# Kernel optimization log

Hardware: AMD Instinct MI355X
Metric: run time of the kernel (lower is better)

Reference implementation:

```python
import jax, jax.numpy as jnp
import numpy as np

NEURONS = 54
DT = 4
STEPS = 30
POOL = 8

# SpikingNN: forward = (ex > 0).float(); backward = straight-through where ex > 0.
# Combined with nn.functional.threshold(rate, thr, 0), the spike output is
# (rate > thr).float() with gradient d spike/d rate = 1{rate > thr}.
@jax.custom_vjp
def spike(rate, thr):
    return (rate > thr).astype(rate.dtype)

def _spike_fwd(rate, thr):
    mask = rate > thr
    return mask.astype(rate.dtype), mask

def _spike_bwd(mask, g):
    return (g * mask.astype(g.dtype), jnp.zeros((), g.dtype))

spike.defvjp(_spike_fwd, _spike_bwd)

def setup_inputs() -> dict:
    key = jax.random.key(0)
    k1, k2, k3, k4, k5 = jax.random.split(key, 5)
    B = 16
    x = jax.random.normal(k1, (B, STEPS, 600, 600), jnp.float32)
    # small scales keep exp(current_sum) numerically stable
    fc_w = jax.random.normal(k2, (NEURONS, 75 * 75), jnp.float32) * 0.01
    fc_b = jax.random.normal(k3, (NEURONS,), jnp.float32) * 0.01
    l_weight = jax.random.uniform(k4, (NEURONS, DT), jnp.float32) * 0.01
    h_weight = jax.random.uniform(k5, (DT,), jnp.float32) * 0.01
    return {"x": x, "fc_w": fc_w, "fc_b": fc_b, "l_weight": l_weight, "h_weight": h_weight}

def reference(x, fc_w, fc_b, l_weight, h_weight):
    B = x.shape[0]
    H = x.shape[2] // POOL
    W = x.shape[3] // POOL
    # avg_pool2d(x, 8): non-overlapping 8x8 mean -> [B, 30, 75, 75]
    xp = x.reshape(B, STEPS, H, POOL, W, POOL).mean(axis=(3, 5))
    # per-frame fc: [B, 30, 5625] @ [5625, 54]^T + b -> [B, 30, 54]
    frames = jnp.einsum('btp,np->btn', xp.reshape(B, STEPS, H * W), fc_w) + fc_b
    count0 = jnp.zeros((B, NEURONS), x.dtype)
    hist0 = jnp.zeros((B, NEURONS, DT), x.dtype)

    def step(carry, frame):
        count, hist = carry                      # hist: [B, N, DT]
        hsum = hist * l_weight                   # [B, N, DT]
        lateral = hsum.sum(axis=(1, 2))[:, None] - hsum.sum(axis=2)  # [B, N]
        cur = frame + lateral + (hist * h_weight).sum(axis=2)
        rate = jnp.exp(cur)
        thr = jax.lax.stop_gradient(rate.mean())
        s = spike(rate, thr)                     # [B, N]
        hist = jnp.concatenate([hist[:, :, 1:], s[:, :, None]], axis=2)
        return (count + s, hist), None

    (count, _), _ = jax.lax.scan(step, (count0, hist0), jnp.swapaxes(frames, 0, 1))
    return jax.nn.softplus(count)
```

## Files before the change

kernel.cpp:

```cpp
#include <hip/hip_runtime.h>
#include <math.h>

#define NEURONS 54
#define DT 4
#define STEPS 30
#define BATCH 16
#define HW 75
#define P 5625
#define PPAD 5632
#define PPAD4 (PPAD/4)

__global__ void repack_w(const float* __restrict__ fc_w, float* __restrict__ wpad) {
    int idx = blockIdx.x * blockDim.x + threadIdx.x;
    if (idx >= NEURONS * PPAD) return;
    int n = idx / PPAD, p = idx % PPAD;
    wpad[idx] = (p < P) ? fc_w[n * P + p] : 0.0f;
}

__global__ __launch_bounds__(512) void pool_fc(
    const float* __restrict__ x, const float* __restrict__ wpad,
    const float* __restrict__ fc_b, float* __restrict__ frames) {
    __shared__ __align__(16) float xp_s[PPAD];
    __shared__ float partial[NEURONS * 8];
    const int bt = blockIdx.x;
    const int tid = threadIdx.x;
    const float* img = x + (size_t)bt * (600 * 600);

    if (tid < PPAD - P) xp_s[P + tid] = 0.0f;

    for (int p = tid; p < P; p += 512) {
        int ph = p / HW, pw = p - ph * HW;
        const float* base = img + (ph * 8) * 600 + pw * 8;
        float acc = 0.0f;
        #pragma unroll
        for (int r = 0; r < 8; r++) {
            const float4* row = (const float4*)(base + r * 600);
            float4 a = row[0], b4 = row[1];
            acc += (a.x + b4.x) + (a.y + b4.y) + (a.z + b4.z) + (a.w + b4.w);
        }
        xp_s[p] = acc * (1.0f / 64.0f);
    }
    __syncthreads();

    if (tid < NEURONS * 8) {
        int n = tid >> 3, c = tid & 7;
        const float4* w4 = (const float4*)(wpad + n * PPAD);
        const float4* x4 = (const float4*)xp_s;
        float acc = 0.0f;
        for (int i = c; i < PPAD4; i += 8) {
            float4 a = x4[i], w = w4[i];
            acc += a.x * w.x + a.y * w.y + a.z * w.z + a.w * w.w;
        }
        partial[tid] = acc;
    }
    __syncthreads();
    if (tid < NEURONS) {
        float s = 0.0f;
        #pragma unroll
        for (int c = 0; c < 8; c++) s += partial[tid * 8 + c];
        frames[bt * NEURONS + tid] = s + fc_b[tid];
    }
}

__global__ __launch_bounds__(1024) void scan_k(
    const float* __restrict__ frames, const float* __restrict__ l_weight,
    const float* __restrict__ h_weight, float* __restrict__ out) {
    const int tid = threadIdx.x;
    const int b = tid >> 6;
    const int n = tid & 63;
    const bool active = (n < NEURONS);

    float lw[DT], hw_[DT];
    #pragma unroll
    for (int d = 0; d < DT; d++) {
        lw[d]  = active ? l_weight[n * DT + d] : 0.0f;
        hw_[d] = h_weight[d];
    }
    float hist[DT] = {0.f, 0.f, 0.f, 0.f};
    float count = 0.f;
    __shared__ float wls[16];

    for (int t = 0; t < STEPS; t++) {
        float my_hsum = 0.f, hterm = 0.f;
        #pragma unroll
        for (int d = 0; d < DT; d++) {
            my_hsum += hist[d] * lw[d];
            hterm   += hist[d] * hw_[d];
        }
        float tot = my_hsum;
        #pragma unroll
        for (int off = 32; off > 0; off >>= 1) tot += __shfl_xor(tot, off, 64);

        float rate = 0.f;
        if (active) {
            float cur = frames[(b * STEPS + t) * NEURONS + n] + (tot - my_hsum) + hterm;
            rate = expf(cur);
        }
        float rsum = rate;
        #pragma unroll
        for (int off = 32; off > 0; off >>= 1) rsum += __shfl_xor(rsum, off, 64);
        __syncthreads();
        if (n == 0) wls[b] = rsum;
        __syncthreads();
        float v = (n < 16) ? wls[n] : 0.f;
        #pragma unroll
        for (int off = 32; off > 0; off >>= 1) v += __shfl_xor(v, off, 64);
        float thr = v * (1.0f / (BATCH * NEURONS));

        float s = (active && rate > thr) ? 1.0f : 0.0f;
        count += s;
        hist[0] = hist[1]; hist[1] = hist[2]; hist[2] = hist[3]; hist[3] = s;
    }
    if (active) {
        out[b * NEURONS + n] = count + log1pf(expf(-count));
    }
}

extern "C" void kernel_launch(void* const* d_in, const int* in_sizes, int n_in,
                              void* d_out, int out_size, void* d_ws, size_t ws_size,
                              hipStream_t stream) {
    const float* x        = (const float*)d_in[0];
    const float* fc_w     = (const float*)d_in[1];
    const float* fc_b     = (const float*)d_in[2];
    const float* l_weight = (const float*)d_in[3];
    const float* h_weight = (const float*)d_in[4];
    float* out = (float*)d_out;

    float* wpad   = (float*)d_ws;
    float* frames = wpad + NEURONS * PPAD;

    int wtotal = NEURONS * PPAD;
    repack_w<<<(wtotal + 511) / 512, 512, 0, stream>>>(fc_w, wpad);
    pool_fc<<<BATCH * STEPS, 512, 0, stream>>>(x, wpad, fc_b, frames);
    scan_k<<<1, 1024, 0, stream>>>(frames, l_weight, h_weight, out);
}
```

Baseline: 943.1 us.

## Split pooling into wide-grid kernel and batch frames in FC kernel

Splits the fused pool+FC kernel into a separate pooling kernel launched on a 2D grid (22 blocks per frame × 480 frames), which writes pooled frames to workspace. A new FC kernel then processes 4 frames per block, so each weight float4 loaded is reused across four frames. The aim is to expose far more parallelism for the bandwidth-bound pooling read of x and to cut repeated weight traffic. In exchange it adds an intermediate global write and read of the pooled frames, an extra launch, and only 120 FC blocks.

```diff
diff --git a/kernel.cpp b/kernel.cpp
--- a/kernel.cpp
+++ b/kernel.cpp
@@ -9,6 +9,8 @@
 #define P 5625
 #define PPAD 5632
 #define PPAD4 (PPAD/4)
+#define NFRAMES (BATCH*STEPS)
+#define FPB 4
 
 __global__ void repack_w(const float* __restrict__ fc_w, float* __restrict__ wpad) {
     int idx = blockIdx.x * blockDim.x + threadIdx.x;
@@ -17,48 +19,63 @@
     wpad[idx] = (p < P) ? fc_w[n * P + p] : 0.0f;
 }
 
-__global__ __launch_bounds__(512) void pool_fc(
-    const float* __restrict__ x, const float* __restrict__ wpad,
+__global__ __launch_bounds__(256) void pool_k(
+    const float* __restrict__ x, float* __restrict__ xp) {
+    const int p  = blockIdx.x * 256 + threadIdx.x;
+    const int bt = blockIdx.y;
+    if (p >= P) {
+        xp[(size_t)bt * PPAD + p] = 0.0f;
+        return;
+    }
+    const int ph = p / HW, pw = p - ph * HW;
+    const float* base = x + (size_t)bt * (600 * 600) + (ph * 8) * 600 + pw * 8;
+    float acc = 0.0f;
+    #pragma unroll
+    for (int r = 0; r < 8; r++) {
+        const float4* row = (const float4*)(base + r * 600);
+        float4 a = row[0], b4 = row[1];
+        acc += (a.x + b4.x) + (a.y + b4.y) + (a.z + b4.z) + (a.w + b4.w);
+    }
+    xp[(size_t)bt * PPAD + p] = acc * (1.0f / 64.0f);
+}
+
+__global__ __launch_bounds__(512) void fc_k(
+    const float* __restrict__ xp, const float* __restrict__ wpad,
     const float* __restrict__ fc_b, float* __restrict__ frames) {
-    __shared__ __align__(16) float xp_s[PPAD];
-    __shared__ float partial[NEURONS * 8];
-    const int bt = blockIdx.x;
+    __shared__ __align__(16) float xs[FPB][PPAD];
+    __shared__ float partial[FPB][NEURONS * 8];
     const int tid = threadIdx.x;
-    const float* img = x + (size_t)bt * (600 * 600);
+    const int f0 = blockIdx.x * FPB;
 
-    if (tid < PPAD - P) xp_s[P + tid] = 0.0f;
+    const float4* src = (const float4*)(xp + (size_t)f0 * PPAD);
+    float4* dst = (float4*)(&xs[0][0]);
+    #pragma unroll
+    for (int i = tid; i < FPB * PPAD4; i += 512) dst[i] = src[i];
+    __syncthreads();
 
-    for (int p = tid; p < P; p += 512) {
-        int ph = p / HW, pw = p - ph * HW;
-        const float* base = img + (ph * 8) * 600 + pw * 8;
-        float acc = 0.0f;
+    if (tid < NEURONS * 8) {
+        const int n = tid >> 3, c = tid & 7;
+        const float4* w4 = (const float4*)(wpad + n * PPAD);
+        float acc[FPB] = {0.f, 0.f, 0.f, 0.f};
+        for (int i = c; i < PPAD4; i += 8) {
+            float4 w = w4[i];
+            #pragma unroll
+            for (int f = 0; f < FPB; f++) {
+                float4 a = ((const float4*)xs[f])[i];
+                acc[f] += a.x * w.x + a.y * w.y + a.z * w.z + a.w * w.w;
+            }
+        }
         #pragma unroll
-        for (int r = 0; r < 8; r++) {
-            const float4* row = (const float4*)(base + r * 600);
-            float4 a = row[0], b4 = row[1];
-            acc += (a.x + b4.x) + (a.y + b4.y) + (a.z + b4.z) + (a.w + b4.w);
-        }
-        xp_s[p] = acc * (1.0f / 64.0f);
+        for (int f = 0; f < FPB; f++) partial[f][tid] = acc[f];
     }
     __syncthreads();
 
-    if (tid < NEURONS * 8) {
-        int n = tid >> 3, c = tid & 7;
-        const float4* w4 = (const float4*)(wpad + n * PPAD);
-        const float4* x4 = (const float4*)xp_s;
-        float acc = 0.0f;
-        for (int i = c; i < PPAD4; i += 8) {
-            float4 a = x4[i], w = w4[i];
-            acc += a.x * w.x + a.y * w.y + a.z * w.z + a.w * w.w;
-        }
-        partial[tid] = acc;
-    }
-    __syncthreads();
-    if (tid < NEURONS) {
+    if (tid < FPB * NEURONS) {
+        const int f = tid / NEURONS, n = tid - f * NEURONS;
         float s = 0.0f;
         #pragma unroll
-        for (int c = 0; c < 8; c++) s += partial[tid * 8 + c];
-        frames[bt * NEURONS + tid] = s + fc_b[tid];
+        for (int c = 0; c < 8; c++) s += partial[f][n * 8 + c];
+        frames[(size_t)(f0 + f) * NEURONS + n] = s + fc_b[n];
     }
 }
 
@@ -127,10 +144,12 @@
     float* out = (float*)d_out;
 
     float* wpad   = (float*)d_ws;
-    float* frames = wpad + NEURONS * PPAD;
+    float* xp     = wpad + NEURONS * PPAD;
+    float* frames = xp + (size_t)NFRAMES * PPAD;
 
     int wtotal = NEURONS * PPAD;
     repack_w<<<(wtotal + 511) / 512, 512, 0, stream>>>(fc_w, wpad);
-    pool_fc<<<BATCH * STEPS, 512, 0, stream>>>(x, wpad, fc_b, frames);
+    pool_k<<<dim3(PPAD / 256, NFRAMES), 256, 0, stream>>>(x, xp);
+    fc_k<<<NFRAMES / FPB, 512, 0, stream>>>(xp, wpad, fc_b, frames);
     scan_k<<<1, 1024, 0, stream>>>(frames, l_weight, h_weight, out);
 }
```

Result: slower. 998.9 us (+5.9%).
